# Optimization experiments

Measured on AMD Instinct MI355X. Metric: run time of the kernel, lower is better.

Reference implementation:

```python
import jax, jax.numpy as jnp
import numpy as np

HIDDEN = 1024
FEAT = 64
BATCH = 512
SEQ = 64
EPS = 1e-5


def _gru_layer(x_seq, Wih, Whh, bih, bhh):
    # x_seq: [B,T,Din]; Wih: [3H,Din]; Whh: [3H,H]; gate order r,z,n (PyTorch)
    B = x_seq.shape[0]
    H = Whh.shape[1]
    gates_x = jnp.einsum('btd,gd->btg', x_seq, Wih) + bih  # [B,T,3H]
    h0 = jnp.zeros((B, H), x_seq.dtype)

    def step(h, gx):
        gh = h @ Whh.T + bhh                       # [B,3H]
        xr, xz, xn = jnp.split(gx, 3, axis=-1)
        hr, hz, hn = jnp.split(gh, 3, axis=-1)
        r = jax.nn.sigmoid(xr + hr)
        z = jax.nn.sigmoid(xz + hz)
        n = jnp.tanh(xn + r * hn)
        h_new = (1.0 - z) * n + z * h
        return h_new, h_new

    _, ys = jax.lax.scan(step, h0, jnp.swapaxes(gates_x, 0, 1))  # [T,B,H]
    return jnp.swapaxes(ys, 0, 1)                                # [B,T,H]


def setup_inputs() -> dict:
    key = jax.random.key(0)
    ks = jax.random.split(key, 20)
    s = 1.0 / np.sqrt(HIDDEN)
    u = lambda k, shape: jax.random.uniform(k, shape, jnp.float32, -s, s)
    inp = {
        'x': jax.random.normal(ks[0], (BATCH, SEQ, FEAT), jnp.float32),
        'Wih0': u(ks[1], (3 * HIDDEN, FEAT)),
        'Whh0': u(ks[2], (3 * HIDDEN, HIDDEN)),
        'bih0': u(ks[3], (3 * HIDDEN,)),
        'bhh0': u(ks[4], (3 * HIDDEN,)),
        'Wih1': u(ks[5], (3 * HIDDEN, HIDDEN)),
        'Whh1': u(ks[6], (3 * HIDDEN, HIDDEN)),
        'bih1': u(ks[7], (3 * HIDDEN,)),
        'bhh1': u(ks[8], (3 * HIDDEN,)),
        'Wih2': u(ks[9], (3 * HIDDEN, HIDDEN)),
        'Whh2': u(ks[10], (3 * HIDDEN, HIDDEN)),
        'bih2': u(ks[11], (3 * HIDDEN,)),
        'bhh2': u(ks[12], (3 * HIDDEN,)),
        'gamma': jnp.ones((HIDDEN,), jnp.float32),
        'beta': jnp.zeros((HIDDEN,), jnp.float32),
        'fcW': u(ks[13], (1, HIDDEN)),
        'fcb': u(ks[14], (1,)),
    }
    return inp


def reference(x, Wih0, Whh0, bih0, bhh0, Wih1, Whh1, bih1, bhh1,
              Wih2, Whh2, bih2, bhh2, gamma, beta, fcW, fcb):
    h = _gru_layer(x, Wih0, Whh0, bih0, bhh0)
    h = _gru_layer(h, Wih1, Whh1, bih1, bhh1)
    h = _gru_layer(h, Wih2, Whh2, bih2, bhh2)
    out = h[:, -1, :]                               # [B,H] last timestep
    # BatchNorm1d in training mode: biased batch stats (B != 1 branch)
    mu = jnp.mean(out, axis=0)
    var = jnp.mean((out - mu) ** 2, axis=0)
    out = (out - mu) * jax.lax.rsqrt(var + EPS) * gamma + beta
    out = out @ fcW.T + fcb                         # [B,1]
    return jax.nn.sigmoid(out)[:, 0]                # [B]
```

## Files before the change

kernel.cpp:

```cpp
#include <hip/hip_runtime.h>
#include <hip/hip_bf16.h>
#include <stdint.h>

#define HIDDEN 1024
#define FEAT   64
#define BATCH  512
#define SEQ    64
#define GATES  3072

typedef __attribute__((ext_vector_type(4))) float f32x4;
typedef __attribute__((ext_vector_type(8))) short s16x8;

#define MFMA16(a, b, c) __builtin_amdgcn_mfma_f32_16x16x32_bf16(a, b, c, 0, 0, 0)
#define VMCNT(n) asm volatile("s_waitcnt vmcnt(" #n ")" ::: "memory")
#define LGKMCNT0 asm volatile("s_waitcnt lgkmcnt(0)" ::: "memory")

__device__ inline unsigned short f2bf(float f) {
    unsigned u = __builtin_bit_cast(unsigned, f);
    u += 0x7fff + ((u >> 16) & 1);
    return (unsigned short)(u >> 16);
}
__device__ inline float bf2f(unsigned short s) {
    unsigned u = ((unsigned)s) << 16;
    return __builtin_bit_cast(float, u);
}

#define GLOAD_LDS16(g, l) __builtin_amdgcn_global_load_lds( \
    (const __attribute__((address_space(1))) unsigned int*)(g), \
    (__attribute__((address_space(3))) unsigned int*)(l), 16, 0, 0)

__global__ void k_conv_whh_t(const float* __restrict__ src, unsigned short* __restrict__ dst) {
    int i = blockIdx.x * 256 + threadIdx.x;
    int ub = i / 49152;
    int r  = i - ub * 49152;
    int c  = r / 3072;
    int r2 = r - c * 3072;
    int srow = r2 >> 6, scol = r2 & 63;
    int src_row = ((srow >> 4) << 10) + (ub << 4) + (srow & 15);
    dst[i] = f2bf(src[(size_t)src_row * 1024 + (c << 6) + scol]);
}

__global__ void k_conv_wih0_t(const float* __restrict__ src, unsigned short* __restrict__ dst) {
    int i = blockIdx.x * 256 + threadIdx.x;
    int ub = i / 3072;
    int r  = i - ub * 3072;
    int srow = r >> 6, scol = r & 63;
    int src_row = ((srow >> 4) << 10) + (ub << 4) + (srow & 15);
    dst[i] = f2bf(src[(size_t)src_row * 64 + scol]);
}

__global__ void k_xpose(const float* __restrict__ x, unsigned short* __restrict__ xbf) {
    int i = blockIdx.x * blockDim.x + threadIdx.x;
    if (i >= BATCH * SEQ * FEAT) return;
    int f = i & 63, t = (i >> 6) & 63, b = i >> 12;
    xbf[((size_t)t * BATCH + b) * FEAT + f] = f2bf(x[i]);
}

__device__ __forceinline__ void stage_pair(const char* ws, const char* as,
                                           unsigned short* Wd, unsigned short* Ad,
                                           int wid, int lane)
{
    const int lrow = lane >> 3;
    const int srcoff = lrow * 128 + (((lane & 7) ^ (lrow & 7)) << 4);
    for (int g = wid; g < 6; g += 4)
        GLOAD_LDS16(ws + (g << 10) + srcoff, (char*)Wd + (g << 10));
#pragma unroll
    for (int r = 0; r < 4; ++r) {
        int g = wid + r * 4;
        GLOAD_LDS16(as + (g << 10) + srcoff, (char*)Ad + (g << 10));
    }
}

template<int NSLOT>
__device__ __forceinline__ void compute_chunk(const unsigned short* aL, const unsigned short* wL,
                                              int wid, int lane, f32x4 (&acc)[2][4])
{
    const int l15 = lane & 15, hi = lane >> 4;
    const int swz = (l15 & 7) << 4;
    const char* ap = (const char*)aL;
    const char* wp = (const char*)wL;
#pragma unroll
    for (int ks = 0; ks < 2; ++ks) {
        const int kb = ks * 64 + (hi << 4);
        s16x8 a0 = *(const s16x8*)(ap + ((((wid * 32 + l15) * 128) + kb) ^ swz));
        s16x8 a1 = *(const s16x8*)(ap + ((((wid * 32 + 16 + l15) * 128) + kb) ^ swz));
        s16x8 b0 = *(const s16x8*)(wp + (((l15 * 128) + kb) ^ swz));
        s16x8 b1 = *(const s16x8*)(wp + ((((16 + l15) * 128) + kb) ^ swz));
        s16x8 b2 = *(const s16x8*)(wp + ((((32 + l15) * 128) + kb) ^ swz));
        acc[0][0]     = MFMA16(a0, b0, acc[0][0]);
        acc[0][1]     = MFMA16(a0, b1, acc[0][1]);
        acc[0][NSLOT] = MFMA16(a0, b2, acc[0][NSLOT]);
        acc[1][0]     = MFMA16(a1, b0, acc[1][0]);
        acc[1][1]     = MFMA16(a1, b1, acc[1][1]);
        acc[1][NSLOT] = MFMA16(a1, b2, acc[1][NSLOT]);
    }
}

__global__ __launch_bounds__(256, 3) void k_stage(
    int d,
    const unsigned short* __restrict__ xbf,
    unsigned short* __restrict__ h0,
    unsigned short* __restrict__ h1,
    unsigned short* __restrict__ h2,
    const unsigned short* __restrict__ wih0R,
    const unsigned short* __restrict__ whh0R,
    const unsigned short* __restrict__ wih1R,
    const unsigned short* __restrict__ whh1R,
    const unsigned short* __restrict__ wih2R,
    const unsigned short* __restrict__ whh2R,
    const float* __restrict__ bih0, const float* __restrict__ bhh0,
    const float* __restrict__ bih1, const float* __restrict__ bhh1,
    const float* __restrict__ bih2, const float* __restrict__ bhh2)
{
    __shared__ unsigned short Wb[2][48 * 64];
    __shared__ unsigned short Ab[2][128 * 64];
    const int bid = blockIdx.x;
    const int slot = bid & 7;
    const int p = (bid >> 3) % 24;
    const int bg = bid / 192;
    const int pair = slot + 8 * p;
    const int layer = pair >> 6;
    const int ub = pair & 63;
    const int t = d - layer;
    if (t < 0 || t >= SEQ) return;

    const int tid = threadIdx.x;
    const int wid = tid >> 6, lane = tid & 63;
    const int l15 = lane & 15, hi = lane >> 4;
    const int brow0 = bg * 128;

    const unsigned short* inseq = (layer == 0) ? xbf : ((layer == 1) ? h0 : h1);
    unsigned short* outseq = (layer == 0) ? h0 : ((layer == 1) ? h1 : h2);
    const unsigned short* wihR = (layer == 0) ? wih0R : ((layer == 1) ? wih1R : wih2R);
    const unsigned short* whhR = (layer == 0) ? whh0R : ((layer == 1) ? whh1R : whh2R);

    const char* a1base = (layer == 0)
        ? (const char*)xbf + (size_t)t * 65536 + (size_t)brow0 * 128
        : (const char*)inseq + (size_t)(t & 1) * 1048576 + (size_t)brow0 * 128;
    const char* w1base = (layer == 0)
        ? (const char*)wih0R + (size_t)ub * 6144
        : (const char*)wihR + (size_t)ub * 98304;
    const char* a2base = (const char*)outseq + (size_t)((t - 1) & 1) * 1048576 + (size_t)brow0 * 128;
    const char* w2base = (const char*)whhR + (size_t)ub * 98304;

    const int NCH1 = (layer == 0) ? 1 : 16;
    const int NCH2 = (t > 0) ? 16 : 0;
    const int total = NCH1 + NCH2;

    auto srcs = [&](int c, const char*& ws, const char*& as) {
        if (c < NCH1) {
            ws = w1base + (size_t)c * 6144;
            as = a1base + (size_t)c * 65536;
        } else {
            int c2 = c - NCH1;
            ws = w2base + (size_t)c2 * 6144;
            as = a2base + (size_t)c2 * 65536;
        }
    };

    f32x4 acc[2][4];
    const f32x4 zero = {0.f, 0.f, 0.f, 0.f};
#pragma unroll
    for (int i = 0; i < 2; ++i)
#pragma unroll
        for (int s = 0; s < 4; ++s) acc[i][s] = zero;

    {
        const char* ws; const char* as;
        srcs(0, ws, as);
        stage_pair(ws, as, Wb[0], Ab[0], wid, lane);
    }

    for (int c = 0; c < total; ++c) {
        const int cb = c & 1;
        if (c + 1 < total) {
            const char* ws; const char* as;
            srcs(c + 1, ws, as);
            stage_pair(ws, as, Wb[cb ^ 1], Ab[cb ^ 1], wid, lane);
            if (wid < 2) VMCNT(6); else VMCNT(5);
        } else {
            VMCNT(0);
        }
        __builtin_amdgcn_s_barrier();
        __builtin_amdgcn_sched_barrier(0);
        if (c < NCH1) compute_chunk<2>(Ab[cb], Wb[cb], wid, lane, acc);
        else          compute_chunk<3>(Ab[cb], Wb[cb], wid, lane, acc);
        LGKMCNT0;
        __builtin_amdgcn_sched_barrier(0);
        __builtin_amdgcn_s_barrier();
    }

    const float* bih = (layer == 0) ? bih0 : ((layer == 1) ? bih1 : bih2);
    const float* bhh = (layer == 0) ? bhh0 : ((layer == 1) ? bhh1 : bhh2);
    const int j = ub * 16 + l15;
    const float br  = bih[j] + bhh[j];
    const float bz  = bih[HIDDEN + j] + bhh[HIDDEN + j];
    const float bxn = bih[2 * HIDDEN + j];
    const float bhn = bhh[2 * HIDDEN + j];
    const unsigned short* hprev = outseq + (size_t)((t > 0) ? ((t - 1) & 1) : 0) * (512 * 1024);
    unsigned short* hout = outseq + (size_t)(t & 1) * (512 * 1024);
    const int jc = (ub >> 2);
    const int jcol = (ub & 3) * 16 + l15;
#pragma unroll
    for (int i = 0; i < 2; ++i)
#pragma unroll
        for (int r = 0; r < 4; ++r) {
            int brow = brow0 + wid * 32 + i * 16 + hi * 4 + r;
            size_t hidx = (size_t)(jc * 512 + brow) * 64 + jcol;
            float rg = 1.f / (1.f + __expf(-(acc[i][0][r] + br)));
            float zg = 1.f / (1.f + __expf(-(acc[i][1][r] + bz)));
            float ng = tanhf(acc[i][2][r] + bxn + rg * (acc[i][3][r] + bhn));
            float hv = (t > 0) ? bf2f(hprev[hidx]) : 0.f;
            float hnew = (1.f - zg) * ng + zg * hv;
            hout[hidx] = f2bf(hnew);
        }
}

__global__ void k_bn_part(const unsigned short* __restrict__ h, float* __restrict__ part) {
    int j = threadIdx.x;
    int blk = blockIdx.x;
    const int jc = j >> 6, jcol = j & 63;
    float s = 0.f, q = 0.f;
    for (int b = blk * 32; b < blk * 32 + 32; ++b) {
        float v = bf2f(h[(size_t)(jc * 512 + b) * 64 + jcol]);
        s += v; q += v * v;
    }
    part[blk * 2048 + j] = s;
    part[blk * 2048 + 1024 + j] = q;
}

__global__ void k_bn_fold(const float* __restrict__ part, const float* __restrict__ gamma,
                          const float* __restrict__ beta, float* __restrict__ a, float* __restrict__ bb)
{
    int j = blockIdx.x * 256 + threadIdx.x;
    float s = 0.f, q = 0.f;
    for (int p = 0; p < 16; ++p) {
        s += part[p * 2048 + j];
        q += part[p * 2048 + 1024 + j];
    }
    float mu = s * (1.f / BATCH);
    float var = q * (1.f / BATCH) - mu * mu;
    float rs = rsqrtf(var + 1e-5f);
    float aj = gamma[j] * rs;
    a[j] = aj;
    bb[j] = beta[j] - mu * aj;
}

__global__ void k_fc(const unsigned short* __restrict__ h, const float* __restrict__ a, const float* __restrict__ bb,
                     const float* __restrict__ fcW, const float* __restrict__ fcb, float* __restrict__ out)
{
    int b = blockIdx.x;
    int lane = threadIdx.x;
    float s = 0.f;
    for (int j = lane; j < HIDDEN; j += 64)
        s += (bf2f(h[(size_t)((j >> 6) * 512 + b) * 64 + (j & 63)]) * a[j] + bb[j]) * fcW[j];
#pragma unroll
    for (int m = 32; m; m >>= 1) s += __shfl_xor(s, m, 64);
    if (lane == 0) out[b] = 1.f / (1.f + __expf(-(s + fcb[0])));
}

extern "C" void kernel_launch(void* const* d_in, const int* in_sizes, int n_in,
                              void* d_out, int out_size, void* d_ws, size_t ws_size,
                              hipStream_t stream)
{
    const float* x = (const float*)d_in[0];
    const float* W_ih[3] = {(const float*)d_in[1], (const float*)d_in[5], (const float*)d_in[9]};
    const float* W_hh[3] = {(const float*)d_in[2], (const float*)d_in[6], (const float*)d_in[10]};
    const float* b_ih[3] = {(const float*)d_in[3], (const float*)d_in[7], (const float*)d_in[11]};
    const float* b_hh[3] = {(const float*)d_in[4], (const float*)d_in[8], (const float*)d_in[12]};
    const float* gamma = (const float*)d_in[13];
    const float* beta  = (const float*)d_in[14];
    const float* fcW   = (const float*)d_in[15];
    const float* fcb   = (const float*)d_in[16];

    char* ws = (char*)d_ws;
    size_t off = 0;
    auto alloc = [&](size_t bytes) -> void* {
        void* p = ws + off;
        off = (off + bytes + 255) & ~(size_t)255;
        return p;
    };
    unsigned short* wih0R = (unsigned short*)alloc((size_t)GATES * FEAT * 2);
    unsigned short* whh0R = (unsigned short*)alloc((size_t)GATES * HIDDEN * 2);
    unsigned short* wih1R = (unsigned short*)alloc((size_t)GATES * HIDDEN * 2);
    unsigned short* whh1R = (unsigned short*)alloc((size_t)GATES * HIDDEN * 2);
    unsigned short* wih2R = (unsigned short*)alloc((size_t)GATES * HIDDEN * 2);
    unsigned short* whh2R = (unsigned short*)alloc((size_t)GATES * HIDDEN * 2);
    unsigned short* xbf = (unsigned short*)alloc((size_t)SEQ * BATCH * FEAT * 2);
    unsigned short* h0  = (unsigned short*)alloc((size_t)2 * BATCH * HIDDEN * 2);
    unsigned short* h1  = (unsigned short*)alloc((size_t)2 * BATCH * HIDDEN * 2);
    unsigned short* h2  = (unsigned short*)alloc((size_t)2 * BATCH * HIDDEN * 2);
    float* part = (float*)alloc(16 * 2048 * 4);
    float* abuf = (float*)alloc(HIDDEN * 4);
    float* bbuf = (float*)alloc(HIDDEN * 4);

    k_conv_wih0_t<<<(GATES * FEAT) / 256, 256, 0, stream>>>(W_ih[0], wih0R);
    k_conv_whh_t<<<(GATES * HIDDEN) / 256, 256, 0, stream>>>(W_hh[0], whh0R);
    k_conv_whh_t<<<(GATES * HIDDEN) / 256, 256, 0, stream>>>(W_ih[1], wih1R);
    k_conv_whh_t<<<(GATES * HIDDEN) / 256, 256, 0, stream>>>(W_hh[1], whh1R);
    k_conv_whh_t<<<(GATES * HIDDEN) / 256, 256, 0, stream>>>(W_ih[2], wih2R);
    k_conv_whh_t<<<(GATES * HIDDEN) / 256, 256, 0, stream>>>(W_hh[2], whh2R);
    k_xpose<<<(BATCH * SEQ * FEAT + 255) / 256, 256, 0, stream>>>(x, xbf);

    for (int d = 0; d < SEQ + 2; ++d)
        k_stage<<<768, 256, 0, stream>>>(d, xbf, h0, h1, h2,
                                         wih0R, whh0R, wih1R, whh1R, wih2R, whh2R,
                                         b_ih[0], b_hh[0], b_ih[1], b_hh[1], b_ih[2], b_hh[2]);

    const unsigned short* hlast = h2 + (size_t)((SEQ - 1) & 1) * (BATCH * HIDDEN);
    k_bn_part<<<16, 1024, 0, stream>>>(hlast, part);
    k_bn_fold<<<HIDDEN / 256, 256, 0, stream>>>(part, gamma, beta, abuf, bbuf);
    k_fc<<<BATCH, 64, 0, stream>>>(hlast, abuf, bbuf, fcW, fcb, (float*)d_out);
}
```

Measured before the change: 2.174 ms.

## Double hidden-unit tile per block to reuse staged activations across two unit groups

Each k_stage block now computes 32 hidden units (two 16-unit groups, 96 gate rows) instead of 16, so each staged activation chunk is reused for twice as many MFMAs. The weight reorder kernels are changed to pack weights in this 32-unit layout, the grid is halved to 384 blocks, and occupancy is lowered to 2 blocks per CU. This cuts activation load traffic per output but doubles accumulator registers and LDS for weights, and leaves fewer blocks to fill the GPU.

```diff
diff --git a/kernel.cpp b/kernel.cpp
--- a/kernel.cpp
+++ b/kernel.cpp
@@ -31,21 +31,25 @@
 
 __global__ void k_conv_whh_t(const float* __restrict__ src, unsigned short* __restrict__ dst) {
     int i = blockIdx.x * 256 + threadIdx.x;
-    int ub = i / 49152;
-    int r  = i - ub * 49152;
-    int c  = r / 3072;
-    int r2 = r - c * 3072;
+    int ub = i / 98304;
+    int r  = i - ub * 98304;
+    int c  = r / 6144;
+    int r2 = r - c * 6144;
     int srow = r2 >> 6, scol = r2 & 63;
-    int src_row = ((srow >> 4) << 10) + (ub << 4) + (srow & 15);
+    int ug = srow / 48, rr = srow - ug * 48;
+    int g = rr >> 4, jj = rr & 15;
+    int src_row = (g << 10) + (ub << 5) + (ug << 4) + jj;
     dst[i] = f2bf(src[(size_t)src_row * 1024 + (c << 6) + scol]);
 }
 
 __global__ void k_conv_wih0_t(const float* __restrict__ src, unsigned short* __restrict__ dst) {
     int i = blockIdx.x * 256 + threadIdx.x;
-    int ub = i / 3072;
-    int r  = i - ub * 3072;
+    int ub = i / 6144;
+    int r  = i - ub * 6144;
     int srow = r >> 6, scol = r & 63;
-    int src_row = ((srow >> 4) << 10) + (ub << 4) + (srow & 15);
+    int ug = srow / 48, rr = srow - ug * 48;
+    int g = rr >> 4, jj = rr & 15;
+    int src_row = (g << 10) + (ub << 5) + (ug << 4) + jj;
     dst[i] = f2bf(src[(size_t)src_row * 64 + scol]);
 }
 
@@ -62,8 +66,11 @@
 {
     const int lrow = lane >> 3;
     const int srcoff = lrow * 128 + (((lane & 7) ^ (lrow & 7)) << 4);
-    for (int g = wid; g < 6; g += 4)
+#pragma unroll
+    for (int r = 0; r < 3; ++r) {
+        int g = wid * 3 + r;
         GLOAD_LDS16(ws + (g << 10) + srcoff, (char*)Wd + (g << 10));
+    }
 #pragma unroll
     for (int r = 0; r < 4; ++r) {
         int g = wid + r * 4;
@@ -73,7 +80,7 @@
 
 template<int NSLOT>
 __device__ __forceinline__ void compute_chunk(const unsigned short* aL, const unsigned short* wL,
-                                              int wid, int lane, f32x4 (&acc)[2][4])
+                                              int wid, int lane, f32x4 (&acc)[2][2][4])
 {
     const int l15 = lane & 15, hi = lane >> 4;
     const int swz = (l15 & 7) << 4;
@@ -84,19 +91,23 @@
         const int kb = ks * 64 + (hi << 4);
         s16x8 a0 = *(const s16x8*)(ap + ((((wid * 32 + l15) * 128) + kb) ^ swz));
         s16x8 a1 = *(const s16x8*)(ap + ((((wid * 32 + 16 + l15) * 128) + kb) ^ swz));
-        s16x8 b0 = *(const s16x8*)(wp + (((l15 * 128) + kb) ^ swz));
-        s16x8 b1 = *(const s16x8*)(wp + ((((16 + l15) * 128) + kb) ^ swz));
-        s16x8 b2 = *(const s16x8*)(wp + ((((32 + l15) * 128) + kb) ^ swz));
-        acc[0][0]     = MFMA16(a0, b0, acc[0][0]);
-        acc[0][1]     = MFMA16(a0, b1, acc[0][1]);
-        acc[0][NSLOT] = MFMA16(a0, b2, acc[0][NSLOT]);
-        acc[1][0]     = MFMA16(a1, b0, acc[1][0]);
-        acc[1][1]     = MFMA16(a1, b1, acc[1][1]);
-        acc[1][NSLOT] = MFMA16(a1, b2, acc[1][NSLOT]);
-    }
-}
-
-__global__ __launch_bounds__(256, 3) void k_stage(
+#pragma unroll
+        for (int ug = 0; ug < 2; ++ug) {
+            const int wr = ug * 48 + l15;
+            s16x8 b0 = *(const s16x8*)(wp + ((((wr)      * 128) + kb) ^ swz));
+            s16x8 b1 = *(const s16x8*)(wp + ((((wr + 16) * 128) + kb) ^ swz));
+            s16x8 b2 = *(const s16x8*)(wp + ((((wr + 32) * 128) + kb) ^ swz));
+            acc[0][ug][0]     = MFMA16(a0, b0, acc[0][ug][0]);
+            acc[0][ug][1]     = MFMA16(a0, b1, acc[0][ug][1]);
+            acc[0][ug][NSLOT] = MFMA16(a0, b2, acc[0][ug][NSLOT]);
+            acc[1][ug][0]     = MFMA16(a1, b0, acc[1][ug][0]);
+            acc[1][ug][1]     = MFMA16(a1, b1, acc[1][ug][1]);
+            acc[1][ug][NSLOT] = MFMA16(a1, b2, acc[1][ug][NSLOT]);
+        }
+    }
+}
+
+__global__ __launch_bounds__(256, 2) void k_stage(
     int d,
     const unsigned short* __restrict__ xbf,
     unsigned short* __restrict__ h0,
@@ -112,15 +123,15 @@
     const float* __restrict__ bih1, const float* __restrict__ bhh1,
     const float* __restrict__ bih2, const float* __restrict__ bhh2)
 {
-    __shared__ unsigned short Wb[2][48 * 64];
+    __shared__ unsigned short Wb[2][96 * 64];
     __shared__ unsigned short Ab[2][128 * 64];
     const int bid = blockIdx.x;
     const int slot = bid & 7;
-    const int p = (bid >> 3) % 24;
-    const int bg = bid / 192;
+    const int p = (bid >> 3) % 12;
+    const int bg = bid / 96;
     const int pair = slot + 8 * p;
-    const int layer = pair >> 6;
-    const int ub = pair & 63;
+    const int layer = pair >> 5;
+    const int ub = pair & 31;
     const int t = d - layer;
     if (t < 0 || t >= SEQ) return;
 
@@ -138,10 +149,10 @@
         ? (const char*)xbf + (size_t)t * 65536 + (size_t)brow0 * 128
         : (const char*)inseq + (size_t)(t & 1) * 1048576 + (size_t)brow0 * 128;
     const char* w1base = (layer == 0)
-        ? (const char*)wih0R + (size_t)ub * 6144
-        : (const char*)wihR + (size_t)ub * 98304;
+        ? (const char*)wih0R + (size_t)ub * 12288
+        : (const char*)wihR + (size_t)ub * 196608;
     const char* a2base = (const char*)outseq + (size_t)((t - 1) & 1) * 1048576 + (size_t)brow0 * 128;
-    const char* w2base = (const char*)whhR + (size_t)ub * 98304;
+    const char* w2base = (const char*)whhR + (size_t)ub * 196608;
 
     const int NCH1 = (layer == 0) ? 1 : 16;
     const int NCH2 = (t > 0) ? 16 : 0;
@@ -149,21 +160,23 @@
 
     auto srcs = [&](int c, const char*& ws, const char*& as) {
         if (c < NCH1) {
-            ws = w1base + (size_t)c * 6144;
+            ws = w1base + (size_t)c * 12288;
             as = a1base + (size_t)c * 65536;
         } else {
             int c2 = c - NCH1;
-            ws = w2base + (size_t)c2 * 6144;
+            ws = w2base + (size_t)c2 * 12288;
             as = a2base + (size_t)c2 * 65536;
         }
     };
 
-    f32x4 acc[2][4];
+    f32x4 acc[2][2][4];
     const f32x4 zero = {0.f, 0.f, 0.f, 0.f};
 #pragma unroll
     for (int i = 0; i < 2; ++i)
 #pragma unroll
-        for (int s = 0; s < 4; ++s) acc[i][s] = zero;
+        for (int ug = 0; ug < 2; ++ug)
+#pragma unroll
+            for (int s = 0; s < 4; ++s) acc[i][ug][s] = zero;
 
     {
         const char* ws; const char* as;
@@ -177,7 +190,7 @@
             const char* ws; const char* as;
             srcs(c + 1, ws, as);
             stage_pair(ws, as, Wb[cb ^ 1], Ab[cb ^ 1], wid, lane);
-            if (wid < 2) VMCNT(6); else VMCNT(5);
+            VMCNT(7);
         } else {
             VMCNT(0);
         }
@@ -192,28 +205,31 @@
 
     const float* bih = (layer == 0) ? bih0 : ((layer == 1) ? bih1 : bih2);
     const float* bhh = (layer == 0) ? bhh0 : ((layer == 1) ? bhh1 : bhh2);
-    const int j = ub * 16 + l15;
-    const float br  = bih[j] + bhh[j];
-    const float bz  = bih[HIDDEN + j] + bhh[HIDDEN + j];
-    const float bxn = bih[2 * HIDDEN + j];
-    const float bhn = bhh[2 * HIDDEN + j];
     const unsigned short* hprev = outseq + (size_t)((t > 0) ? ((t - 1) & 1) : 0) * (512 * 1024);
     unsigned short* hout = outseq + (size_t)(t & 1) * (512 * 1024);
-    const int jc = (ub >> 2);
-    const int jcol = (ub & 3) * 16 + l15;
-#pragma unroll
-    for (int i = 0; i < 2; ++i)
-#pragma unroll
-        for (int r = 0; r < 4; ++r) {
-            int brow = brow0 + wid * 32 + i * 16 + hi * 4 + r;
-            size_t hidx = (size_t)(jc * 512 + brow) * 64 + jcol;
-            float rg = 1.f / (1.f + __expf(-(acc[i][0][r] + br)));
-            float zg = 1.f / (1.f + __expf(-(acc[i][1][r] + bz)));
-            float ng = tanhf(acc[i][2][r] + bxn + rg * (acc[i][3][r] + bhn));
-            float hv = (t > 0) ? bf2f(hprev[hidx]) : 0.f;
-            float hnew = (1.f - zg) * ng + zg * hv;
-            hout[hidx] = f2bf(hnew);
-        }
+    const int jc = ub >> 1;
+#pragma unroll
+    for (int ug = 0; ug < 2; ++ug) {
+        const int j = ub * 32 + ug * 16 + l15;
+        const int jcol = (ub & 1) * 32 + ug * 16 + l15;
+        const float br  = bih[j] + bhh[j];
+        const float bz  = bih[HIDDEN + j] + bhh[HIDDEN + j];
+        const float bxn = bih[2 * HIDDEN + j];
+        const float bhn = bhh[2 * HIDDEN + j];
+#pragma unroll
+        for (int i = 0; i < 2; ++i)
+#pragma unroll
+            for (int r = 0; r < 4; ++r) {
+                int brow = brow0 + wid * 32 + i * 16 + hi * 4 + r;
+                size_t hidx = (size_t)(jc * 512 + brow) * 64 + jcol;
+                float rg = 1.f / (1.f + __expf(-(acc[i][ug][0][r] + br)));
+                float zg = 1.f / (1.f + __expf(-(acc[i][ug][1][r] + bz)));
+                float ng = tanhf(acc[i][ug][2][r] + bxn + rg * (acc[i][ug][3][r] + bhn));
+                float hv = (t > 0) ? bf2f(hprev[hidx]) : 0.f;
+                float hnew = (1.f - zg) * ng + zg * hv;
+                hout[hidx] = f2bf(hnew);
+            }
+    }
 }
 
 __global__ void k_bn_part(const unsigned short* __restrict__ h, float* __restrict__ part) {
@@ -303,7 +319,7 @@
     k_xpose<<<(BATCH * SEQ * FEAT + 255) / 256, 256, 0, stream>>>(x, xbf);
 
     for (int d = 0; d < SEQ + 2; ++d)
-        k_stage<<<768, 256, 0, stream>>>(d, xbf, h0, h1, h2,
+        k_stage<<<384, 256, 0, stream>>>(d, xbf, h0, h1, h2,
                                          wih0R, whh0R, wih1R, whh1R, wih2R, whh2R,
                                          b_ih[0], b_hh[0], b_ih[1], b_hh[1], b_ih[2], b_hh[2]);
 
```

After: 2.530 ms. 1.16x slower.
